# Optimization experiments

Hardware: AMD Instinct MI355X
Metric: run time of the kernel (lower is better)

Reference implementation:

```python
import jax, jax.numpy as jnp
import numpy as np

B, S, D = 8, 1024, 768          # batch, block_size, d_model
H = 6                            # n_head
E = 24                           # n_experts
CAP = 4                          # n_expert_capacity
DH = D // H                      # 128, head dim
DF = 384                         # d_ffn
N = S * H                        # tokens after head split = 6144
K = N * CAP // E                 # tokens per expert = 1024


def _uniform(key, shape, fan_in):
    b = 1.0 / np.sqrt(fan_in)
    return jax.random.uniform(key, shape, jnp.float32, -b, b)


def setup_inputs() -> dict:
    key = jax.random.key(0)
    kx, kc, k1, k2, kh, km = jax.random.split(key, 6)
    return {
        "x": jax.random.normal(kx, (B, S, D), jnp.float32),
        "choice": _uniform(kc, (E, DH), DH),
        "w1": _uniform(k1, (E, DH, DF), DH),
        "w2": _uniform(k2, (E, DF, DH), DF),
        "head": _uniform(kh, (D, D), D),
        "merge": _uniform(km, (D, D), D),
    }


def reference(x, choice, w1, w2, head, merge):
    Bb = x.shape[0]
    # input projection then split heads into a token stream of length N
    x = jnp.einsum("bsd,do->bso", x, head)
    x = x.reshape(Bb, N, DH)                              # [B, N, DH]
    # expert-choice routing: softmax over experts per token
    gates = jax.nn.softmax(jnp.einsum("bsd,ed->bse", x, choice), axis=-1)
    # each expert picks its top-K tokens
    G, I = jax.lax.top_k(jnp.swapaxes(gates, -1, -2), K)  # [B, E, K]
    bidx = jnp.arange(Bb)[:, None, None]
    # gather (equivalent to one-hot matmul einsum('beks,bsd->bekd', P, x))
    x_in = x[bidx, I]                                     # [B, E, K, DH]
    # per-expert SwiGLU-free FFN: silu(x w1) w2
    h = jax.nn.silu(jnp.einsum("bekd,edo->beko", x_in, w1))
    x_mlp = jnp.einsum("beki,eid->bekd", h, w2)           # [B, E, K, DH]
    # scatter-combine weighted by gates (einsum('beks,bek,bekd->bsd'))
    x_out = jnp.zeros((Bb, N, DH), x.dtype).at[bidx, I].add(G[..., None] * x_mlp)
    # dropout is identity in eval mode
    x_out = x_out.reshape(Bb, S, D)
    return jnp.einsum("bsd,do->bso", x_out, merge)
```

## Files before the change

### kernel.cpp

```cpp
#include <hip/hip_runtime.h>
#include <stdint.h>
#include <math.h>

typedef __attribute__((ext_vector_type(8))) short short8;
typedef __attribute__((ext_vector_type(4))) short short4v;
typedef __attribute__((ext_vector_type(4))) float floatx4;
typedef __attribute__((ext_vector_type(2))) float floatx2;

#define DEV static __device__ __forceinline__

DEV float bf2f(unsigned short u){ union { unsigned int i; float f; } c; c.i = ((unsigned int)u) << 16; return c.f; }
DEV unsigned short f2bf(float f){ union { float f; unsigned int i; } c; c.f = f; unsigned int u = c.i; u += 0x7fffu + ((u >> 16) & 1u); return (unsigned short)(u >> 16); }

#if defined(__has_builtin)
#if __has_builtin(__builtin_amdgcn_global_load_lds)
#define USE_GLL 1
#endif
#if __has_builtin(__builtin_amdgcn_exp2f) && __has_builtin(__builtin_amdgcn_rcpf)
#define FAST_SILU 1
#endif
#endif
#ifndef USE_GLL
#define USE_GLL 0
#endif
#ifndef FAST_SILU
#define FAST_SILU 0
#endif

DEV void gll16(const unsigned short* g, unsigned short* ldsbase, int lane){
#if USE_GLL
  __builtin_amdgcn_global_load_lds((const __attribute__((address_space(1))) void*)g,
                                   (__attribute__((address_space(3))) void*)ldsbase, 16, 0, 0);
#else
  *(short8*)(ldsbase + lane * 8) = *(const short8*)g;
#endif
}

DEV float silu(float v){
#if FAST_SILU
  float ex = __builtin_amdgcn_exp2f(v * -1.44269504088896f);
  return v * __builtin_amdgcn_rcpf(1.f + ex);
#else
  return v / (1.f + __expf(-v));
#endif
}

DEV void transpose_tile(const float* in, unsigned short* out, int R, int C,
                        int bx, int by, int bz, int tid, unsigned short* tile)
{
  const long boff = (long)bz * (long)R * (long)C;
  in += boff; out += boff;
  const int c0 = bx * 64, r0 = by * 64;
  const int rr = tid >> 4;
  const int c4 = (tid & 15) * 4;
#pragma unroll
  for (int i = 0; i < 4; i++){
    int r = rr + i * 16;
    floatx4 v = *(const floatx4*)(in + (long)(r0 + r) * C + c0 + c4);
#pragma unroll
    for (int u = 0; u < 4; u++) tile[r * 68 + c4 + u] = f2bf(v[u]);
  }
  __syncthreads();
#pragma unroll
  for (int i = 0; i < 4; i++){
    int cc = rr + i * 16;
    short4v v;
#pragma unroll
    for (int u = 0; u < 4; u++) v[u] = (short)tile[(c4 + u) * 68 + cc];
    *(short4v*)(out + (long)(c0 + cc) * R + r0 + c4) = v;
  }
}

__global__ __launch_bounds__(256) void k_prep(const float* __restrict__ x,
    const float* __restrict__ choice, const float* __restrict__ w1,
    const float* __restrict__ w2, const float* __restrict__ head,
    const float* __restrict__ merge,
    unsigned short* __restrict__ xb, unsigned short* __restrict__ headT,
    unsigned short* __restrict__ mergeT, unsigned short* __restrict__ w1T,
    unsigned short* __restrict__ w2T, double* __restrict__ W64)
{
  __shared__ double buf[1536];
  unsigned short* tile = (unsigned short*)buf;
  const int id = blockIdx.x, tid = threadIdx.x;
  if (id < 144){
    transpose_tile(head, headT, 768, 768, id % 12, id / 12, 0, tid, tile);
  } else if (id < 288){
    int l = id - 144;
    transpose_tile(merge, mergeT, 768, 768, l % 12, l / 12, 0, tid, tile);
  } else if (id < 576){
    int l = id - 288;
    transpose_tile(w1, w1T, 128, 384, l % 6, (l / 6) % 2, l / 12, tid, tile);
  } else if (id < 864){
    int l = id - 576;
    transpose_tile(w2, w2T, 384, 128, l % 2, (l / 2) % 6, l / 12, tid, tile);
  } else if (id < 1248){
    int l = id - 864;
    const int sub = tid >> 7, lt = tid & 127;
    const int d = l * 2 + sub;
    double* hrow = buf + sub * 768;
    for (int i = lt; i < 768; i += 128) hrow[i] = (double)head[(long)d * 768 + i];
    __syncthreads();
    for (int c = lt; c < 144; c += 128){
      int h = c / 24, e = c % 24;
      double a = 0.0;
      const double* hr = hrow + h * 128;
      const float* ch = choice + e * 128;
#pragma unroll 8
      for (int k = 0; k < 128; k++) a += hr[k] * (double)ch[k];
      W64[(long)d * 144 + c] = a;
    }
  } else {
    const long l = id - 1248;
    const long i = (l * 256 + tid) * 4;
    floatx4 v = *(const floatx4*)(x + i);
    short4v o;
#pragma unroll
    for (int u = 0; u < 4; u++) o[u] = (short)f2bf(v[u]);
    *(short4v*)(xb + i) = o;
  }
}

template<int OUTF>
DEV void gemm_body(const unsigned short* __restrict__ A, const unsigned short* __restrict__ BT,
                   unsigned short* __restrict__ C, float* __restrict__ Cf, int N, int K,
                   unsigned short* As, unsigned short* Bs, int m0, int n0, int tid)
{
  const int lane = tid & 63;
  const int w = tid >> 6;
  const int wy = w >> 1, wx = w & 1;

  floatx4 acc[4][4];
  {
    floatx4 z4 = {0.f, 0.f, 0.f, 0.f};
#pragma unroll
    for (int i = 0; i < 4; i++)
#pragma unroll
      for (int j = 0; j < 4; j++) acc[i][j] = z4;
  }

  const int rsub = lane >> 3;
  const int kcol = (lane & 7) * 8;

  for (int k0 = 0; k0 < K; k0 += 64){
#pragma unroll
    for (int i = 0; i < 4; i++){
      const int inst = w * 4 + i;
      const int rr = inst * 8 + rsub;
      gll16(A + (long)(m0 + rr) * K + k0 + kcol, &As[inst * 512], lane);
      gll16(BT + (long)(n0 + rr) * K + k0 + kcol, &Bs[inst * 512], lane);
    }
    __syncthreads();
#pragma unroll
    for (int ks = 0; ks < 2; ++ks){
      const int kb = ks * 32 + (lane >> 4) * 8;
      short8 af[4], bfr[4];
#pragma unroll
      for (int mi = 0; mi < 4; mi++) af[mi]  = *(const short8*)&As[(wy * 64 + mi * 16 + (lane & 15)) * 64 + kb];
#pragma unroll
      for (int ni = 0; ni < 4; ni++) bfr[ni] = *(const short8*)&Bs[(wx * 64 + ni * 16 + (lane & 15)) * 64 + kb];
#pragma unroll
      for (int mi = 0; mi < 4; mi++)
#pragma unroll
        for (int ni = 0; ni < 4; ni++)
          acc[mi][ni] = __builtin_amdgcn_mfma_f32_16x16x32_bf16(af[mi], bfr[ni], acc[mi][ni], 0, 0, 0);
    }
    __syncthreads();
  }

  const int ml = lane & 15;
  const int rq = (lane >> 4) * 4;
#pragma unroll
  for (int mi = 0; mi < 4; mi++){
    const int rowb = m0 + wy * 64 + mi * 16 + rq;
#pragma unroll
    for (int ni = 0; ni < 4; ni++){
      const int col = n0 + wx * 64 + ni * 16 + ml;
#pragma unroll
      for (int r = 0; r < 4; r++){
        float v = acc[mi][ni][r];
        if (OUTF) Cf[(long)(rowb + r) * N + col] = v;
        else      C[(long)(rowb + r) * N + col] = f2bf(v);
      }
    }
  }
}

DEV void gates_body(const float* __restrict__ xg, const double* __restrict__ W,
                    double* __restrict__ P, float* xs, double* Ws,
                    int row0, int ksegIdx, int tid)
{
  const int tx = tid & 15;
  const int ty = tid >> 4;
  const int kseg = ksegIdx * 192;

  double acc[2][9];
#pragma unroll
  for (int i = 0; i < 2; i++)
#pragma unroll
    for (int j = 0; j < 9; j++) acc[i][j] = 0.0;

  for (int kc = 0; kc < 192; kc += 32){
    const int k0 = kseg + kc;
    {
      int rr = tid & 31;
      int kk4 = (tid >> 5) * 4;
      floatx4 v = *(const floatx4*)(xg + (long)(row0 + rr) * 768 + k0 + kk4);
#pragma unroll
      for (int u = 0; u < 4; u++) xs[(kk4 + u) * 32 + rr] = v[u];
    }
    for (int f = tid; f < 4608; f += 256) Ws[f] = W[(long)(k0 + f / 144) * 144 + (f % 144)];
    __syncthreads();
#pragma unroll 2
    for (int kk = 0; kk < 32; kk++){
      floatx2 xv = *(const floatx2*)&xs[kk * 32 + ty * 2];
      double x0 = (double)xv[0], x1d = (double)xv[1];
#pragma unroll
      for (int j = 0; j < 9; j++){
        double wv = Ws[kk * 144 + tx + 16 * j];
        acc[0][j] += x0 * wv;
        acc[1][j] += x1d * wv;
      }
    }
    __syncthreads();
  }
  double* dstseg = P + (long)ksegIdx * 8192 * 144;
#pragma unroll
  for (int i = 0; i < 2; i++){
    double* dst = dstseg + (long)(row0 + ty * 2 + i) * 144;
#pragma unroll
    for (int j = 0; j < 9; j++) dst[tx + 16 * j] = acc[i][j];
  }
}

__global__ __launch_bounds__(256, 4) void k_main0(const unsigned short* __restrict__ xb,
    const unsigned short* __restrict__ headT, unsigned short* __restrict__ x1,
    const float* __restrict__ xg, const double* __restrict__ W, double* __restrict__ P)
{
  __shared__ double lds[5120];
  const int id = blockIdx.x, tid = threadIdx.x;
  if (id < 1024){
    float* xs = (float*)lds;
    double* Ws = (double*)((char*)lds + 4096);
    gates_body(xg, W, P, xs, Ws, (id & 255) * 32, id >> 8, tid);
  } else {
    const int id2 = id - 1024;
    unsigned short* As = (unsigned short*)lds;
    unsigned short* Bs = As + 128 * 64;
    gemm_body<0>(xb, headT, x1, nullptr, 768, 768, As, Bs, (id2 & 63) * 128, (id2 >> 6) * 128, tid);
  }
}

__global__ __launch_bounds__(256) void k_softmax(const double* __restrict__ P,
                                                 double* __restrict__ gatesT)
{
  const int gid = blockIdx.x * 256 + threadIdx.x;
  const int R = gid / 6, h = gid % 6;
  const int b = R >> 10, s = R & 1023;
  const int n = s * 6 + h;
  const long S = (long)8192 * 144;
  const long base = (long)R * 144 + h * 24;
  double l[24];
#pragma unroll
  for (int e = 0; e < 24; e++){
    const long o = base + e;
    l[e] = (P[o] + P[S + o]) + (P[2 * S + o] + P[3 * S + o]);
  }
  double m = l[0];
#pragma unroll
  for (int e = 1; e < 24; e++) m = fmax(m, l[e]);
  double ssum = 0.0;
#pragma unroll
  for (int e = 0; e < 24; e++){ l[e] = exp(l[e] - m); ssum += l[e]; }
  double is = 1.0 / ssum;
#pragma unroll
  for (int e = 0; e < 24; e++)
    gatesT[((long)(b * 24 + e)) * 6144 + n] = l[e] * is;
}

DEV int blk_reduce(int v, volatile int* sbuf, int tid){
#pragma unroll
  for (int off = 32; off > 0; off >>= 1) v += __shfl_down(v, off);
  __syncthreads();
  if ((tid & 63) == 0) sbuf[tid >> 6] = v;
  __syncthreads();
  return sbuf[0] + sbuf[1] + sbuf[2] + sbuf[3];
}

__global__ __launch_bounds__(256) void k_topk(const double* __restrict__ gatesT,
                                              int* __restrict__ Kidx, float* __restrict__ Gval,
                                              int* __restrict__ cnt, unsigned short* __restrict__ inv)
{
  __shared__ int sbuf[4];
  __shared__ int s_pos;
  const int tid = threadIdx.x;
  const int be = blockIdx.x;
  const int b = be / 24, e = be % 24;
  const double* g = gatesT + (long)be * 6144;

  unsigned long long key[24];
#pragma unroll
  for (int j = 0; j < 24; j++)
    key[j] = (unsigned long long)__double_as_longlong(g[tid + 256 * j]);

  unsigned long long lo = 0ull, hi = ~0ull;
  for (int it = 0; it < 64; ++it){
    if (hi - lo <= 1ull) break;
    unsigned long long mid = lo + ((hi - lo) >> 1);
    int c = 0;
#pragma unroll
    for (int j = 0; j < 24; j++) c += (key[j] > mid) ? 1 : 0;
    c = blk_reduce(c, sbuf, tid);
    if (c >= 1024) lo = mid; else hi = mid;
  }
  const unsigned long long T = hi;
  int cg = 0;
#pragma unroll
  for (int j = 0; j < 24; j++) cg += (key[j] > T) ? 1 : 0;
  cg = blk_reduce(cg, sbuf, tid);
  const int need = 1024 - cg;

  int lo2 = 0, hi2 = 6144;
  for (int it = 0; it < 13; ++it){
    if (hi2 - lo2 <= 1) break;
    int mid = (lo2 + hi2) >> 1;
    int c = 0;
#pragma unroll
    for (int j = 0; j < 24; j++) c += (key[j] == T && (tid + 256 * j) < mid) ? 1 : 0;
    c = blk_reduce(c, sbuf, tid);
    if (c >= need) hi2 = mid; else lo2 = mid;
  }
  const int m = hi2;

  if (tid == 0) s_pos = 0;
  __syncthreads();
#pragma unroll
  for (int j = 0; j < 24; j++){
    int n = tid + 256 * j;
    bool sel = (key[j] > T) || (key[j] == T && n < m);
    if (sel){
      int slot = atomicAdd(&s_pos, 1);
      Kidx[(long)be * 1024 + slot] = n;
      Gval[(long)be * 1024 + slot] = (float)__longlong_as_double((long long)key[j]);
      int t = b * 6144 + n;
      int p = atomicAdd(&cnt[t], 1);
      inv[(long)t * 24 + p] = (unsigned short)(e * 1024 + slot);
    }
  }
}

__global__ __launch_bounds__(256, 2) void k_gemm2(const unsigned short* __restrict__ A,
    const unsigned short* __restrict__ BT, float* __restrict__ Cf)
{
  __shared__ unsigned short As[128 * 64];
  __shared__ unsigned short Bs[128 * 64];
  gemm_body<1>(A, BT, nullptr, Cf, 768, 768, As, Bs,
               (int)blockIdx.x * 128, (int)blockIdx.y * 128, (int)threadIdx.x);
}

__global__ __launch_bounds__(256, 2) void k_ffn(const unsigned short* __restrict__ x1,
    const unsigned short* __restrict__ w1T, const unsigned short* __restrict__ w2T,
    const int* __restrict__ KidxAll, const float* __restrict__ GvalAll,
    unsigned short* __restrict__ Y)
{
  __shared__ unsigned short As[128 * 128];
  __shared__ unsigned short W1c[64 * 128];
  __shared__ unsigned short W2c[128 * 64];
  __shared__ unsigned short Hc[128 * 64];
  const int tid = threadIdx.x, lane = tid & 63, w = tid >> 6;
  const int tx = lane & 15, quad = lane >> 4;
  const int mt = blockIdx.x;
  const int be = blockIdx.y;
  const int b = be / 24, e = be % 24;
  const int* idx = KidxAll + (long)be * 1024 + mt * 128;
  const float* scl = GvalAll + (long)be * 1024 + mt * 128;
  const unsigned short* A   = x1  + (long)b * 6144 * 128;
  const unsigned short* w1e = w1T + (long)e * 384 * 128;
  const unsigned short* w2e = w2T + (long)e * 128 * 384;

  {
    const int r0 = w * 32;
#pragma unroll
    for (int i = 0; i < 8; i++){
      int rr = r0 + i * 4 + quad;
      int c = tx ^ (rr & 15);
      gll16(A + (long)idx[rr] * 128 + c * 8, &As[(r0 + i * 4) * 128], lane);
    }
  }

  floatx4 Yt[2][8];
  {
    floatx4 z4 = {0.f, 0.f, 0.f, 0.f};
#pragma unroll
    for (int i = 0; i < 2; i++)
#pragma unroll
      for (int j = 0; j < 8; j++) Yt[i][j] = z4;
  }

  for (int nc = 0; nc < 6; ++nc){
    {
      const int r0 = w * 16;
#pragma unroll
      for (int i = 0; i < 4; i++){
        int lr = r0 + i * 4 + quad;
        int c = tx ^ (lr & 15);
        gll16(w1e + (long)(nc * 64 + lr) * 128 + c * 8, &W1c[(r0 + i * 4) * 128], lane);
      }
    }
    {
      const int r0 = w * 32;
#pragma unroll
      for (int i = 0; i < 4; i++){
        int rr = r0 + i * 8 + (lane >> 3);
        int c = (lane & 7) ^ (rr & 7);
        gll16(w2e + (long)rr * 384 + nc * 64 + c * 8, &W2c[(r0 + i * 8) * 64], lane);
      }
    }
    __syncthreads();

    floatx4 h4[2][4];
    {
      floatx4 z4 = {0.f, 0.f, 0.f, 0.f};
#pragma unroll
      for (int i = 0; i < 2; i++)
#pragma unroll
        for (int j = 0; j < 4; j++) h4[i][j] = z4;
    }
#pragma unroll
    for (int ks = 0; ks < 4; ++ks){
      const int chunk = ks * 4 + quad;
      const int pos = chunk ^ tx;
      short8 af[2];
#pragma unroll
      for (int mi = 0; mi < 2; ++mi)
        af[mi] = *(const short8*)&As[(w * 32 + mi * 16 + tx) * 128 + pos * 8];
#pragma unroll
      for (int nf = 0; nf < 4; ++nf){
        short8 bfr = *(const short8*)&W1c[(nf * 16 + tx) * 128 + pos * 8];
#pragma unroll
        for (int mi = 0; mi < 2; ++mi)
          h4[mi][nf] = __builtin_amdgcn_mfma_f32_16x16x32_bf16(af[mi], bfr, h4[mi][nf], 0, 0, 0);
      }
    }
#pragma unroll
    for (int mi = 0; mi < 2; ++mi){
#pragma unroll
      for (int nf = 0; nf < 4; ++nf){
        const int hchunk = nf * 2 + (tx >> 3);
        const int hoff = tx & 7;
#pragma unroll
        for (int r = 0; r < 4; r++){
          float v = silu(h4[mi][nf][r]);
          const int trow = w * 32 + mi * 16 + quad * 4 + r;
          Hc[trow * 64 + (hchunk ^ (trow & 7)) * 8 + hoff] = f2bf(v);
        }
      }
    }
    __syncthreads();

#pragma unroll
    for (int ks = 0; ks < 2; ++ks){
      const int chunk2 = ks * 4 + quad;
      const int posx = chunk2 ^ (tx & 7);
      short8 a2[2], b2[8];
#pragma unroll
      for (int mf = 0; mf < 2; ++mf)
        a2[mf] = *(const short8*)&W2c[(w * 32 + mf * 16 + tx) * 64 + posx * 8];
#pragma unroll
      for (int nf = 0; nf < 8; ++nf)
        b2[nf] = *(const short8*)&Hc[(nf * 16 + tx) * 64 + posx * 8];
#pragma unroll
      for (int mf = 0; mf < 2; ++mf)
#pragma unroll
        for (int nf = 0; nf < 8; ++nf)
          Yt[mf][nf] = __builtin_amdgcn_mfma_f32_16x16x32_bf16(a2[mf], b2[nf], Yt[mf][nf], 0, 0, 0);
    }
    __syncthreads();
  }

#pragma unroll
  for (int nf = 0; nf < 8; ++nf){
    const int rb = nf * 16 + tx;
    const float g = scl[rb];
    unsigned short* dst = Y + ((long)be * 1024 + mt * 128 + rb) * 128 + w * 32 + quad * 4;
#pragma unroll
    for (int mf = 0; mf < 2; ++mf){
      short4v v;
#pragma unroll
      for (int r = 0; r < 4; r++) v[r] = (short)f2bf(Yt[mf][nf][r] * g);
      *(short4v*)(dst + mf * 16) = v;
    }
  }
}

__global__ __launch_bounds__(256) void k_combine(const int* __restrict__ cnt,
    const unsigned short* __restrict__ inv, const unsigned short* __restrict__ Y,
    unsigned short* __restrict__ xout)
{
  const int t = blockIdx.x * 4 + (threadIdx.x >> 6);
  const int lane = threadIdx.x & 63;
  const int b = t / 6144;
  const int c = cnt[t];
  float a0 = 0.f, a1 = 0.f;
  for (int p = 0; p < c; ++p){
    int code = inv[(long)t * 24 + p];
    int e = code >> 10, slot = code & 1023;
    const unsigned short* y = Y + (((long)(b * 24 + e) * 1024 + slot) << 7) + lane * 2;
    a0 += bf2f(y[0]); a1 += bf2f(y[1]);
  }
  unsigned short* o = xout + ((long)t << 7) + lane * 2;
  o[0] = f2bf(a0); o[1] = f2bf(a1);
}

extern "C" void kernel_launch(void* const* d_in, const int* in_sizes, int n_in,
                              void* d_out, int out_size, void* d_ws, size_t ws_size,
                              hipStream_t stream)
{
  const float* x      = (const float*)d_in[0];
  const float* choice = (const float*)d_in[1];
  const float* w1     = (const float*)d_in[2];
  const float* w2     = (const float*)d_in[3];
  const float* head   = (const float*)d_in[4];
  const float* merge  = (const float*)d_in[5];
  float* out = (float*)d_out;
  (void)in_sizes; (void)n_in; (void)out_size; (void)ws_size;

  char* p = (char*)d_ws;
  auto alloc = [&p](size_t bytes) -> void* {
    void* q = (void*)p; p += (bytes + 255) & ~(size_t)255; return q;
  };

  unsigned short* headT = (unsigned short*)alloc((size_t)768 * 768 * 2);
  unsigned short* mergeT= (unsigned short*)alloc((size_t)768 * 768 * 2);
  unsigned short* w1T   = (unsigned short*)alloc((size_t)24 * 384 * 128 * 2);
  unsigned short* w2T   = (unsigned short*)alloc((size_t)24 * 128 * 384 * 2);
  double* W64           = (double*)alloc((size_t)768 * 144 * 8);
  int* Kidx             = (int*)alloc((size_t)192 * 1024 * 4);
  float* Gval           = (float*)alloc((size_t)192 * 1024 * 4);
  int* cnt              = (int*)alloc((size_t)49152 * 4);
  unsigned short* inv   = (unsigned short*)alloc((size_t)49152 * 24 * 2);
  unsigned short* xb    = (unsigned short*)alloc((size_t)8192 * 768 * 2);
  unsigned short* x1    = (unsigned short*)alloc((size_t)8192 * 768 * 2);
  unsigned short* Y     = (unsigned short*)alloc((size_t)192 * 1024 * 128 * 2);
  double* P             = (double*)Y;
  double* gatesT        = (double*)((char*)Y + (size_t)4 * 8192 * 144 * 8);
  unsigned short* xout  = xb;

  hipMemsetAsync(cnt, 0, (size_t)49152 * 4, stream);
  k_prep<<<dim3(7392), 256, 0, stream>>>(x, choice, w1, w2, head, merge,
                                         xb, headT, mergeT, w1T, w2T, W64);
  k_main0<<<dim3(1408), 256, 0, stream>>>(xb, headT, x1, x, W64, P);
  k_softmax<<<dim3(192), 256, 0, stream>>>(P, gatesT);
  k_topk<<<dim3(192), 256, 0, stream>>>(gatesT, Kidx, Gval, cnt, inv);
  k_ffn<<<dim3(8, 192, 1), 256, 0, stream>>>(x1, w1T, w2T, Kidx, Gval, Y);
  k_combine<<<dim3(12288), 256, 0, stream>>>(cnt, inv, Y, xout);
  k_gemm2<<<dim3(64, 6, 1), 256, 0, stream>>>(xout, mergeT, out);
}
```

Measured before the change: 383.6 us.

## Compute FP64 routing gate logits with MFMA f64 instructions instead of scalar FMAs

Replaces the LDS-tiled scalar double-precision gate-logit GEMM with per-wave MFMA f64 16x16x4 accumulation that reads operands straight from global memory, halving the gates block count. A small runtime probe block in the prep kernel discovers the MFMA operand and output lane layout and writes it to scratch, and the gates kernel uses it to map lanes to rows and columns. This aims to cut the FP64 FMA cost of the routing logits while keeping double precision for top-k stability. It adds uncached-looking global loads, scattered 8-byte stores, and a dependency on the probe's layout inference.

```diff
diff --git a/kernel.cpp b/kernel.cpp
--- a/kernel.cpp
+++ b/kernel.cpp
@@ -6,6 +6,7 @@
 typedef __attribute__((ext_vector_type(4))) short short4v;
 typedef __attribute__((ext_vector_type(4))) float floatx4;
 typedef __attribute__((ext_vector_type(2))) float floatx2;
+typedef __attribute__((ext_vector_type(4))) double double4v;
 
 #define DEV static __device__ __forceinline__
 
@@ -77,7 +78,8 @@
     const float* __restrict__ merge,
     unsigned short* __restrict__ xb, unsigned short* __restrict__ headT,
     unsigned short* __restrict__ mergeT, unsigned short* __restrict__ w1T,
-    unsigned short* __restrict__ w2T, double* __restrict__ W64)
+    unsigned short* __restrict__ w2T, double* __restrict__ W64,
+    unsigned int* __restrict__ probe)
 {
   __shared__ double buf[1536];
   unsigned short* tile = (unsigned short*)buf;
@@ -109,7 +111,7 @@
       for (int k = 0; k < 128; k++) a += hr[k] * (double)ch[k];
       W64[(long)d * 144 + c] = a;
     }
-  } else {
+  } else if (id < 7392){
     const long l = id - 1248;
     const long i = (l * 256 + tid) * 4;
     floatx4 v = *(const floatx4*)(x + i);
@@ -117,6 +119,26 @@
 #pragma unroll
     for (int u = 0; u < 4; u++) o[u] = (short)f2bf(v[u]);
     *(short4v*)(xb + i) = o;
+  } else {
+    if (tid < 64){
+      double4v z = {0.0, 0.0, 0.0, 0.0};
+      double4v d1 = __builtin_amdgcn_mfma_f64_16x16x4f64((double)tid, 1.0, z, 0, 0, 0);
+      double4v d2 = __builtin_amdgcn_mfma_f64_16x16x4f64(1.0, (double)tid, z, 0, 0, 0);
+      const int V0 = (int)d1[0];
+      const int Astd = ((V0 & 3) == 0) ? 1 : 0;
+      unsigned int rp = 0;
+      int V;
+      V = (int)d1[0]; rp |= (unsigned int)(Astd ? (V - 96) >> 2 : (V - 6) >> 4);
+      V = (int)d1[1]; rp |= (unsigned int)(Astd ? (V - 96) >> 2 : (V - 6) >> 4) << 8;
+      V = (int)d1[2]; rp |= (unsigned int)(Astd ? (V - 96) >> 2 : (V - 6) >> 4) << 16;
+      V = (int)d1[3]; rp |= (unsigned int)(Astd ? (V - 96) >> 2 : (V - 6) >> 4) << 24;
+      const int W0 = (int)d2[0];
+      const int Bstd = ((W0 & 3) == 0) ? 1 : 0;
+      const int cl = Bstd ? (W0 - 96) >> 2 : (W0 - 6) >> 4;
+      probe[tid] = rp;
+      probe[64 + tid] = (unsigned int)cl;
+      if (tid == 0) probe[128] = (unsigned int)(Astd | (Bstd << 1));
+    }
   }
 }
 
@@ -185,66 +207,63 @@
   }
 }
 
-DEV void gates_body(const float* __restrict__ xg, const double* __restrict__ W,
-                    double* __restrict__ P, float* xs, double* Ws,
-                    int row0, int ksegIdx, int tid)
-{
-  const int tx = tid & 15;
-  const int ty = tid >> 4;
-  const int kseg = ksegIdx * 192;
-
-  double acc[2][9];
-#pragma unroll
-  for (int i = 0; i < 2; i++)
-#pragma unroll
-    for (int j = 0; j < 9; j++) acc[i][j] = 0.0;
-
-  for (int kc = 0; kc < 192; kc += 32){
-    const int k0 = kseg + kc;
-    {
-      int rr = tid & 31;
-      int kk4 = (tid >> 5) * 4;
-      floatx4 v = *(const floatx4*)(xg + (long)(row0 + rr) * 768 + k0 + kk4);
-#pragma unroll
-      for (int u = 0; u < 4; u++) xs[(kk4 + u) * 32 + rr] = v[u];
-    }
-    for (int f = tid; f < 4608; f += 256) Ws[f] = W[(long)(k0 + f / 144) * 144 + (f % 144)];
-    __syncthreads();
-#pragma unroll 2
-    for (int kk = 0; kk < 32; kk++){
-      floatx2 xv = *(const floatx2*)&xs[kk * 32 + ty * 2];
-      double x0 = (double)xv[0], x1d = (double)xv[1];
-#pragma unroll
-      for (int j = 0; j < 9; j++){
-        double wv = Ws[kk * 144 + tx + 16 * j];
-        acc[0][j] += x0 * wv;
-        acc[1][j] += x1d * wv;
-      }
-    }
-    __syncthreads();
-  }
-  double* dstseg = P + (long)ksegIdx * 8192 * 144;
-#pragma unroll
-  for (int i = 0; i < 2; i++){
-    double* dst = dstseg + (long)(row0 + ty * 2 + i) * 144;
-#pragma unroll
-    for (int j = 0; j < 9; j++) dst[tx + 16 * j] = acc[i][j];
+DEV void gates_mfma(const float* __restrict__ xg, const double* __restrict__ W,
+                    double* __restrict__ P, const unsigned int* __restrict__ probe,
+                    int id, int tid)
+{
+  const int lane = tid & 63, w = tid >> 6;
+  const unsigned int flags = probe[128];
+  const int Astd = (int)(flags & 1u), Bstd = (int)((flags >> 1) & 1u);
+  const unsigned int rp = probe[lane];
+  const int cl = (int)probe[64 + lane];
+  const int ar = Astd ? (lane & 15) : (lane >> 2);
+  const int ak = Astd ? (lane >> 4) : (lane & 3);
+  const int bk = Bstd ? (lane >> 4) : (lane & 3);
+  const int bj = Bstd ? (lane & 15) : (lane >> 2);
+
+  const int kseg = id >> 7;
+  const int row0 = (id & 127) * 64 + w * 16;
+
+  double4v acc[9];
+#pragma unroll
+  for (int t = 0; t < 9; t++) acc[t] = (double4v){0.0, 0.0, 0.0, 0.0};
+
+  const float* arow = xg + (long)(row0 + ar) * 768;
+  const int kbase = kseg * 192;
+  for (int kc = 0; kc < 192; kc += 4){
+    const int k0 = kbase + kc;
+    const double a = (double)arow[k0 + ak];
+    const double* wr = W + (long)(k0 + bk) * 144 + bj;
+#pragma unroll
+    for (int t = 0; t < 9; t++)
+      acc[t] = __builtin_amdgcn_mfma_f64_16x16x4f64(a, wr[t * 16], acc[t], 0, 0, 0);
+  }
+
+  const int r0_ = (int)(rp & 255u), r1_ = (int)((rp >> 8) & 255u);
+  const int r2_ = (int)((rp >> 16) & 255u), r3_ = (int)((rp >> 24) & 255u);
+  double* dst = P + (long)kseg * 8192 * 144 + (long)row0 * 144;
+#pragma unroll
+  for (int t = 0; t < 9; t++){
+    const int cb = t * 16 + cl;
+    dst[(long)r0_ * 144 + cb] = acc[t][0];
+    dst[(long)r1_ * 144 + cb] = acc[t][1];
+    dst[(long)r2_ * 144 + cb] = acc[t][2];
+    dst[(long)r3_ * 144 + cb] = acc[t][3];
   }
 }
 
 __global__ __launch_bounds__(256, 4) void k_main0(const unsigned short* __restrict__ xb,
     const unsigned short* __restrict__ headT, unsigned short* __restrict__ x1,
-    const float* __restrict__ xg, const double* __restrict__ W, double* __restrict__ P)
-{
-  __shared__ double lds[5120];
+    const float* __restrict__ xg, const double* __restrict__ W, double* __restrict__ P,
+    const unsigned int* __restrict__ probe)
+{
+  __shared__ unsigned short lds[128 * 64 * 2];
   const int id = blockIdx.x, tid = threadIdx.x;
-  if (id < 1024){
-    float* xs = (float*)lds;
-    double* Ws = (double*)((char*)lds + 4096);
-    gates_body(xg, W, P, xs, Ws, (id & 255) * 32, id >> 8, tid);
+  if (id < 512){
+    gates_mfma(xg, W, P, probe, id, tid);
   } else {
-    const int id2 = id - 1024;
-    unsigned short* As = (unsigned short*)lds;
+    const int id2 = id - 512;
+    unsigned short* As = lds;
     unsigned short* Bs = As + 128 * 64;
     gemm_body<0>(xb, headT, x1, nullptr, 768, 768, As, Bs, (id2 & 63) * 128, (id2 >> 6) * 128, tid);
   }
@@ -544,11 +563,12 @@
   double* P             = (double*)Y;
   double* gatesT        = (double*)((char*)Y + (size_t)4 * 8192 * 144 * 8);
   unsigned short* xout  = xb;
+  unsigned int* probe   = (unsigned int*)Kidx;
 
   hipMemsetAsync(cnt, 0, (size_t)49152 * 4, stream);
-  k_prep<<<dim3(7392), 256, 0, stream>>>(x, choice, w1, w2, head, merge,
-                                         xb, headT, mergeT, w1T, w2T, W64);
-  k_main0<<<dim3(1408), 256, 0, stream>>>(xb, headT, x1, x, W64, P);
+  k_prep<<<dim3(7393), 256, 0, stream>>>(x, choice, w1, w2, head, merge,
+                                         xb, headT, mergeT, w1T, w2T, W64, probe);
+  k_main0<<<dim3(896), 256, 0, stream>>>(xb, headT, x1, x, W64, P, probe);
   k_softmax<<<dim3(192), 256, 0, stream>>>(P, gatesT);
   k_topk<<<dim3(192), 256, 0, stream>>>(gatesT, Kidx, Gval, cnt, inv);
   k_ffn<<<dim3(8, 192, 1), 256, 0, stream>>>(x1, w1T, w2T, Kidx, Gval, Y);
```

After: 348.9 us. -9.0%, faster.
